# Optimization experiments

Hardware: AMD Instinct MI355X
Metric: run time of the kernel (lower is better)

The kernel has to match this reference:

```python
import jax, jax.numpy as jnp
import numpy as np

H = 256  # hidden_size == in_size
M = int(H * 4 / 3)  # 341, gated-MLP intermediate
EPS = 1e-5


def _layer_norm(x, w, b):
    mu = jnp.mean(x, axis=-1, keepdims=True)
    var = jnp.var(x, axis=-1, keepdims=True)
    return (x - mu) * jax.lax.rsqrt(var + EPS) * w + b


def setup_inputs() -> dict:
    key = jax.random.key(0)
    ks = jax.random.split(key, 8)
    s = 0.02
    inp = {
        "x": jax.random.normal(ks[0], (64, 2048, H), dtype=jnp.float32),
        "ln1_w": jnp.ones((H,), jnp.float32),
        "ln1_b": jnp.zeros((H,), jnp.float32),
        # sLSTM: stacked [z, i, f, o] input and recurrent weights
        "W": jax.random.normal(ks[1], (4 * H, H), jnp.float32) * s,
        "R": jax.random.normal(ks[2], (4 * H, H), jnp.float32) * s,
        "b": jnp.zeros((4 * H,), jnp.float32),
        "up_W": jax.random.normal(ks[3], (M, H), jnp.float32) * s,
        "up_b": jnp.zeros((M,), jnp.float32),
        "gate_W": jax.random.normal(ks[4], (M, H), jnp.float32) * s,
        "gate_b": jnp.zeros((M,), jnp.float32),
        "down_W": jax.random.normal(ks[5], (H, M), jnp.float32) * s,
        "down_b": jnp.zeros((H,), jnp.float32),
        "ln2_w": jnp.ones((H,), jnp.float32),
        "ln2_b": jnp.zeros((H,), jnp.float32),
    }
    return inp


def _slstm(nx, W, R, b):
    # nx: (B, T, H) -> all hidden states (B, T, H)
    B, T, _ = nx.shape
    xW = jnp.einsum("bth,gh->btg", nx, W) + b  # (B, T, 4H)
    xW = jnp.swapaxes(xW, 0, 1)  # (T, B, 4H)

    def step(carry, xw_t):
        h, c, n, m = carry  # each (B, H)
        pre = xw_t + h @ R.T
        z = jnp.tanh(pre[:, :H])
        log_i = pre[:, H:2 * H]
        log_f = pre[:, 2 * H:3 * H]
        o = jax.nn.sigmoid(pre[:, 3 * H:])
        m_new = jnp.maximum(log_f + m, log_i)  # stabilizer
        i_g = jnp.exp(log_i - m_new)
        f_g = jnp.exp(log_f + m - m_new)
        c = f_g * c + i_g * z
        n = f_g * n + i_g
        h = o * (c / n)
        return (h, c, n, m_new), h

    z0 = jnp.zeros((B, H), nx.dtype)
    (_, _, _, _), hs = jax.lax.scan(step, (z0, z0, z0, z0), xW)
    return jnp.swapaxes(hs, 0, 1)  # (B, T, H)


def reference(x, ln1_w, ln1_b, W, R, b, up_W, up_b, gate_W, gate_b,
              down_W, down_b, ln2_w, ln2_b):
    residual = x
    nx = _layer_norm(x, ln1_w, ln1_b)
    lstm_out = _slstm(nx, W, R, b)
    gate_signal = jax.nn.gelu(jnp.einsum("bth,mh->btm", lstm_out, gate_W) + gate_b)
    mlp_inter = jnp.einsum("bth,mh->btm", lstm_out, up_W) + up_b
    mlp_out = jnp.einsum("btm,hm->bth", gate_signal * mlp_inter, down_W) + down_b
    return _layer_norm(mlp_out, ln2_w, ln2_b) + residual
```

## Files before the change

### kernel.cpp

```cpp
#include <hip/hip_runtime.h>
#include <hip/hip_bf16.h>
#include <hip/hip_fp16.h>

typedef _Float16 f16;
typedef __hip_bfloat16 bf16;
typedef short bf16x8 __attribute__((ext_vector_type(8)));
typedef float f32x4 __attribute__((ext_vector_type(4)));
typedef int i32x4 __attribute__((ext_vector_type(4)));
typedef _Float16 f16x2 __attribute__((ext_vector_type(2)));

#define HDIM 256
#define G4   1024
#define TT   2048
#define NB   64
#define NTOK (64*2048)
#define MPAD 384

__device__ __forceinline__ float gelu_tanh(float x) {
    float x3 = x*x*x;
    float t = tanhf(0.7978845608028654f * (x + 0.044715f * x3));
    return 0.5f * x * (1.0f + t);
}

__global__ void k_prep_w(const float* __restrict__ W, bf16* __restrict__ Wb) {
    int i = blockIdx.x*256 + threadIdx.x;
    Wb[i] = __float2bfloat16(W[i]);
}

__global__ __launch_bounds__(256) void k_prep_r8(const float* __restrict__ R,
        char* __restrict__ R8, float* __restrict__ rscale) {
    int wave = threadIdx.x >> 6, lane = threadIdx.x & 63;
    int g = blockIdx.x*4 + wave;
    float4 v = ((const float4*)(R + (long)g*256))[lane];
    float mx = fmaxf(fmaxf(fabsf(v.x), fabsf(v.y)), fmaxf(fabsf(v.z), fabsf(v.w)));
    #pragma unroll
    for (int m = 1; m < 64; m <<= 1) mx = fmaxf(mx, __shfl_xor(mx, m, 64));
    float inv = (mx > 0.f) ? 127.f/mx : 0.f;
    int q0 = (int)rintf(v.x*inv), q1 = (int)rintf(v.y*inv);
    int q2 = (int)rintf(v.z*inv), q3 = (int)rintf(v.w*inv);
    unsigned packed = (q0 & 0xff) | ((q1 & 0xff) << 8) | ((q2 & 0xff) << 16) | ((q3 & 0xff) << 24);
    ((unsigned*)(R8 + (long)g*256))[lane] = packed;
    if (lane == 0) rscale[g] = mx * (1.0f/127.f);
}

__global__ void k_prep_gu(const float* __restrict__ gW, const float* __restrict__ uW,
                          const float* __restrict__ gb, const float* __restrict__ ub,
                          bf16* __restrict__ gWb, bf16* __restrict__ uWb,
                          float* __restrict__ gbp, float* __restrict__ ubp) {
    int i = blockIdx.x*256 + threadIdx.x;
    int r = i >> 8, c = i & 255;
    gWb[i] = __float2bfloat16(r < 341 ? gW[r*256 + c] : 0.f);
    uWb[i] = __float2bfloat16(r < 341 ? uW[r*256 + c] : 0.f);
    if (i < 384) {
        gbp[i] = i < 341 ? gb[i] : 0.f;
        ubp[i] = i < 341 ? ub[i] : 0.f;
    }
}

__global__ void k_prep_down(const float* __restrict__ dW, bf16* __restrict__ dWb) {
    int i = blockIdx.x*256 + threadIdx.x;
    int r = i / 384, c = i % 384;
    dWb[i] = __float2bfloat16(c < 341 ? dW[r*341 + c] : 0.f);
}

__global__ __launch_bounds__(256) void k_ln1(const float* __restrict__ x,
        const float* __restrict__ w, const float* __restrict__ b,
        bf16* __restrict__ nx) {
    int wave = threadIdx.x >> 6, lane = threadIdx.x & 63;
    long tok = (long)blockIdx.x * 4 + wave;
    float4 v = ((const float4*)(x + tok*HDIM))[lane];
    float s = v.x + v.y + v.z + v.w;
    float q = v.x*v.x + v.y*v.y + v.z*v.z + v.w*v.w;
    #pragma unroll
    for (int m = 1; m < 64; m <<= 1) { s += __shfl_xor(s, m, 64); q += __shfl_xor(q, m, 64); }
    float mean = s * (1.0f/HDIM);
    float rs = rsqrtf(q*(1.0f/HDIM) - mean*mean + 1e-5f);
    float4 wv = ((const float4*)w)[lane];
    float4 bv = ((const float4*)b)[lane];
    bf16 tmp[4];
    tmp[0] = __float2bfloat16((v.x-mean)*rs*wv.x + bv.x);
    tmp[1] = __float2bfloat16((v.y-mean)*rs*wv.y + bv.y);
    tmp[2] = __float2bfloat16((v.z-mean)*rs*wv.z + bv.z);
    tmp[3] = __float2bfloat16((v.w-mean)*rs*wv.w + bv.w);
    *(ushort4*)(nx + tok*HDIM + lane*4) = *(ushort4*)tmp;
}

__global__ __launch_bounds__(256) void k_ln2(const f16* __restrict__ mlp,
        const float* __restrict__ x, const float* __restrict__ w,
        const float* __restrict__ b, float* __restrict__ out) {
    int wave = threadIdx.x >> 6, lane = threadIdx.x & 63;
    long tok = (long)blockIdx.x * 4 + wave;
    const f16* mr = mlp + tok*HDIM + lane*4;
    float4 v; v.x = (float)mr[0]; v.y = (float)mr[1]; v.z = (float)mr[2]; v.w = (float)mr[3];
    float s = v.x + v.y + v.z + v.w;
    float q = v.x*v.x + v.y*v.y + v.z*v.z + v.w*v.w;
    #pragma unroll
    for (int m = 1; m < 64; m <<= 1) { s += __shfl_xor(s, m, 64); q += __shfl_xor(q, m, 64); }
    float mean = s * (1.0f/HDIM);
    float rs = rsqrtf(q*(1.0f/HDIM) - mean*mean + 1e-5f);
    float4 wv = ((const float4*)w)[lane];
    float4 bv = ((const float4*)b)[lane];
    float4 xv = ((const float4*)(x + tok*HDIM))[lane];
    float4 ov;
    ov.x = (v.x-mean)*rs*wv.x + bv.x + xv.x;
    ov.y = (v.y-mean)*rs*wv.y + bv.y + xv.y;
    ov.z = (v.z-mean)*rs*wv.z + bv.z + xv.z;
    ov.w = (v.w-mean)*rs*wv.w + bv.w + xv.w;
    ((float4*)(out + tok*HDIM))[lane] = ov;
}

enum { MODE_F16 = 0, MODE_GELU_F16 = 1, MODE_MUL_BF16 = 2, MODE_XW_F16 = 3 };

template<int MODE>
__global__ __launch_bounds__(256) void k_gemm(
    const bf16* __restrict__ A, const bf16* __restrict__ Bm,
    const float* __restrict__ bias, void* __restrict__ Cv,
    const f16* __restrict__ gatebuf,
    int K, int lda, int ldb, int ldc, int ldg)
{
    __shared__ char Al[128*128];
    __shared__ char Bl[64*128];
    const int tid = threadIdx.x;
    const long bm = (long)blockIdx.x * 128;
    const int bn = blockIdx.y * 64;
    const int wave = tid >> 6, lane = tid & 63;
    const int wm = wave >> 1, wn = wave & 1;
    const int l16 = lane & 15, lq = lane >> 4;
    f32x4 acc[4][2] = {};
    for (int k0 = 0; k0 < K; k0 += 64) {
        #pragma unroll
        for (int p = 0; p < 4; ++p) {
            int ci = tid + p*256;
            int row = ci >> 3, s = ci & 7;
            uint4 d = *(const uint4*)(A + (bm + row)*lda + k0 + s*8);
            *(uint4*)(Al + row*128 + ((s ^ (row&7))<<4)) = d;
        }
        #pragma unroll
        for (int p = 0; p < 2; ++p) {
            int ci = tid + p*256;
            int row = ci >> 3, s = ci & 7;
            uint4 d = *(const uint4*)(Bm + (long)(bn + row)*ldb + k0 + s*8);
            *(uint4*)(Bl + row*128 + ((s ^ (row&7))<<4)) = d;
        }
        __syncthreads();
        #pragma unroll
        for (int kc = 0; kc < 2; ++kc) {
            bf16x8 bf[2];
            #pragma unroll
            for (int fn = 0; fn < 2; ++fn) {
                int row = wn*32 + fn*16 + l16;
                int slot = (kc<<2) + lq;
                bf[fn] = *(const bf16x8*)(Bl + row*128 + ((slot ^ (row&7))<<4));
            }
            #pragma unroll
            for (int fm = 0; fm < 4; ++fm) {
                int row = wm*64 + fm*16 + l16;
                int slot = (kc<<2) + lq;
                bf16x8 af = *(const bf16x8*)(Al + row*128 + ((slot ^ (row&7))<<4));
                acc[fm][0] = __builtin_amdgcn_mfma_f32_16x16x32_bf16(af, bf[0], acc[fm][0], 0,0,0);
                acc[fm][1] = __builtin_amdgcn_mfma_f32_16x16x32_bf16(af, bf[1], acc[fm][1], 0,0,0);
            }
        }
        __syncthreads();
    }
    #pragma unroll
    for (int fm = 0; fm < 4; ++fm) {
        #pragma unroll
        for (int fn = 0; fn < 2; ++fn) {
            int n = bn + wn*32 + fn*16 + l16;
            float bv = bias[n];
            #pragma unroll
            for (int r = 0; r < 4; ++r) {
                long m = bm + wm*64 + fm*16 + lq*4 + r;
                float v = acc[fm][fn][r] + bv;
                if constexpr (MODE == MODE_F16) {
                    ((f16*)Cv)[m*ldc + n] = (f16)v;
                } else if constexpr (MODE == MODE_XW_F16) {
                    ((f16*)Cv)[m*ldc + ((n & 255) << 2) + (n >> 8)] = (f16)v;
                } else if constexpr (MODE == MODE_GELU_F16) {
                    ((f16*)Cv)[m*ldc + n] = (f16)gelu_tanh(v);
                } else {
                    float g = (float)gatebuf[m*ldg + n];
                    ((bf16*)Cv)[m*ldc + n] = __float2bfloat16(g * v);
                }
            }
        }
    }
}


__global__ __launch_bounds__(1024) __attribute__((amdgpu_waves_per_eu(4, 4)))
void k_scan(const f16* __restrict__ xW, const char* __restrict__ R8,
            const float* __restrict__ rscale, bf16* __restrict__ h_out)
{
    __shared__ char hq[2][256];
    const int tid = threadIdx.x;
    const int b    = blockIdx.x;
    const int w    = tid >> 6;
    const int lane = tid & 63;
    const int c    = lane & 15;
    const int q    = lane >> 4;
    const int j    = w*16 + c;

    uint4 Bf[4][4];
    #pragma unroll
    for (int m = 0; m < 4; ++m) {
        #pragma unroll
        for (int kk = 0; kk < 4; ++kk)
            Bf[m][kk] = *(const uint4*)(R8 + (long)(j + 256*m)*256 + kk*64 + q*16);
    }
    float rs[4];
    #pragma unroll
    for (int m = 0; m < 4; ++m)
        rs[m] = rscale[j + 256*m] * (1.0f/127.0f);
    if (tid < 64) ((unsigned*)hq[0])[tid] = 0u;

    const char* xg = (const char*)xW + (long)b * TT * 2048 + j*8;
    bf16* hrow = h_out + (long)b * TT * HDIM;

    uint2 XA = *(const uint2*)(xg);
    uint2 XB = *(const uint2*)(xg + 2048);
    float cst = 0.f, nst = 0.f, mst = 0.f;
    int cur = 0;
    __syncthreads();

#define SCAN_STEP(XREG, TPRE)                                                   \
    do {                                                                        \
        f16x2 xlo = __builtin_bit_cast(f16x2, XREG.x);                          \
        f16x2 xhi = __builtin_bit_cast(f16x2, XREG.y);                          \
        XREG = *(const uint2*)(xg + (long)(TPRE)*2048);                         \
        i32x4 af[4];                                                            \
        _Pragma("unroll")                                                       \
        for (int kk = 0; kk < 4; ++kk)                                          \
            af[kk] = __builtin_bit_cast(i32x4,                                  \
                         *(const uint4*)(hq[cur] + kk*64 + q*16));              \
        i32x4 ac0 = {0,0,0,0}, ac1 = {0,0,0,0}, ac2 = {0,0,0,0}, ac3 = {0,0,0,0}; \
        _Pragma("unroll")                                                       \
        for (int kk = 0; kk < 4; ++kk) {                                        \
            ac0 = __builtin_amdgcn_mfma_i32_16x16x64_i8(af[kk], __builtin_bit_cast(i32x4, Bf[0][kk]), ac0, 0,0,0); \
            ac1 = __builtin_amdgcn_mfma_i32_16x16x64_i8(af[kk], __builtin_bit_cast(i32x4, Bf[1][kk]), ac1, 0,0,0); \
            ac2 = __builtin_amdgcn_mfma_i32_16x16x64_i8(af[kk], __builtin_bit_cast(i32x4, Bf[2][kk]), ac2, 0,0,0); \
            ac3 = __builtin_amdgcn_mfma_i32_16x16x64_i8(af[kk], __builtin_bit_cast(i32x4, Bf[3][kk]), ac3, 0,0,0); \
        }                                                                       \
        float pz = rs[0]*(float)ac0[0] + (float)xlo[0];                         \
        float pi = rs[1]*(float)ac1[0] + (float)xlo[1];                         \
        float pf = rs[2]*(float)ac2[0] + (float)xhi[0];                         \
        float po = rs[3]*(float)ac3[0] + (float)xhi[1];                         \
        float e = __expf(-2.0f * fabsf(pz));                                    \
        float z = copysignf((1.0f - e) / (1.0f + e), pz);                       \
        float o = 1.0f / (1.0f + __expf(-po));                                  \
        float mn = fmaxf(pf + mst, pi);                                         \
        float ig = __expf(pi - mn);                                             \
        float fg = __expf(pf + mst - mn);                                       \
        cst = fg*cst + ig*z;                                                    \
        nst = fg*nst + ig;                                                      \
        mst = mn;                                                               \
        float h = o * (cst / nst);                                              \
        if (q == 0) {                                                           \
            hq[cur^1][j] = (char)(int)rintf(h * 127.f);                         \
            hrow[j] = __float2bfloat16(h);                                      \
        }                                                                       \
        __builtin_amdgcn_sched_barrier(0);                                      \
        asm volatile("s_waitcnt lgkmcnt(0)" ::: "memory");                      \
        __builtin_amdgcn_s_barrier();                                           \
        __builtin_amdgcn_sched_barrier(0);                                      \
        cur ^= 1;                                                               \
        hrow += HDIM;                                                           \
    } while (0)

    for (int t = 0; t < TT; t += 2) {
        SCAN_STEP(XA, t + 2);
        SCAN_STEP(XB, t + 3);
    }
#undef SCAN_STEP
}

extern "C" void kernel_launch(void* const* d_in, const int* in_sizes, int n_in,
                              void* d_out, int out_size, void* d_ws, size_t ws_size,
                              hipStream_t stream) {
    const float* x     = (const float*)d_in[0];
    const float* ln1w  = (const float*)d_in[1];
    const float* ln1b  = (const float*)d_in[2];
    const float* W     = (const float*)d_in[3];
    const float* R     = (const float*)d_in[4];
    const float* bg    = (const float*)d_in[5];
    const float* upW   = (const float*)d_in[6];
    const float* upb   = (const float*)d_in[7];
    const float* gateW = (const float*)d_in[8];
    const float* gateb = (const float*)d_in[9];
    const float* downW = (const float*)d_in[10];
    const float* downb = (const float*)d_in[11];
    const float* ln2w  = (const float*)d_in[12];
    const float* ln2b  = (const float*)d_in[13];

    char* ws = (char*)d_ws;
    size_t off = 0;
    auto alloc = [&](size_t bytes) { char* p = ws + off; off += (bytes + 255) & ~255ULL; return p; };
    f16*  mlp16   = (f16*)alloc((size_t)NTOK*HDIM*2);
    char* regionB = alloc((size_t)NTOK*G4*2);
    bf16* h       = (bf16*)alloc((size_t)NTOK*HDIM*2);
    bf16* Wb      = (bf16*)alloc(262144*2);
    char* R8      = (char*)alloc(262144);
    float* rscale = (float*)alloc(1024*4);
    bf16* gWb     = (bf16*)alloc((size_t)MPAD*256*2);
    bf16* uWb     = (bf16*)alloc((size_t)MPAD*256*2);
    bf16* dWb     = (bf16*)alloc((size_t)256*MPAD*2);
    float* gbp    = (float*)alloc(MPAD*4);
    float* ubp    = (float*)alloc(MPAD*4);

    bf16* nx       = (bf16*)mlp16;
    f16*  xWb      = (f16*)regionB;
    f16*  gate_out = (f16*)regionB;
    bf16* prod     = (bf16*)(regionB + (size_t)NTOK*MPAD*2);

    k_prep_w   <<<1024, 256, 0, stream>>>(W, Wb);
    k_prep_r8  <<<256, 256, 0, stream>>>(R, R8, rscale);
    k_prep_gu  <<<384, 256, 0, stream>>>(gateW, upW, gateb, upb, gWb, uWb, gbp, ubp);
    k_prep_down<<<384, 256, 0, stream>>>(downW, dWb);
    k_ln1      <<<NTOK/4, 256, 0, stream>>>(x, ln1w, ln1b, nx);
    k_gemm<MODE_XW_F16><<<dim3(1024, 16), 256, 0, stream>>>(nx, Wb, bg, xWb, nullptr, 256, 256, 256, 1024, 0);
    k_scan     <<<64, 1024, 0, stream>>>(xWb, R8, rscale, h);
    k_gemm<MODE_GELU_F16><<<dim3(1024, 6), 256, 0, stream>>>(h, gWb, gbp, gate_out, nullptr, 256, 256, 256, MPAD, 0);
    k_gemm<MODE_MUL_BF16><<<dim3(1024, 6), 256, 0, stream>>>(h, uWb, ubp, prod, gate_out, 256, 256, 256, MPAD, MPAD);
    k_gemm<MODE_F16><<<dim3(1024, 4), 256, 0, stream>>>(prod, dWb, downb, mlp16, nullptr, MPAD, MPAD, MPAD, HDIM, 0);
    k_ln2      <<<NTOK/4, 256, 0, stream>>>(mlp16, x, ln2w, ln2b, (float*)d_out);
}
```

Before: 2.566 ms.

## Split scan recurrent matvec between MFMA waves and VALU dot4 waves

The recurrent int8 matvec in the sLSTM scan is now divided within each block. Waves 0-7 compute hidden units 0-127 with int8 MFMA as before. Waves 8-15 compute units 128-255 with VALU sdot4 instructions and a DPP quad reduction, and MFMA sections get raised priority via setprio. The aim is to relieve contention on the shared matrix unit, since all 16 waves previously issued MFMAs every step and the per-step latency is the critical path. The cost is that the VALU half may be slower per step, and since both halves meet at a barrier every step, the slower path sets the pace.

```diff
diff --git a/kernel.cpp b/kernel.cpp
--- a/kernel.cpp
+++ b/kernel.cpp
@@ -15,6 +15,27 @@
 #define NB   64
 #define NTOK (64*2048)
 #define MPAD 384
+
+__device__ __forceinline__ int dot4i(unsigned a, unsigned b, int c) {
+#if __has_builtin(__builtin_amdgcn_sdot4)
+    return __builtin_amdgcn_sdot4((int)a, (int)b, c, false);
+#else
+    char4 x = __builtin_bit_cast(char4, a), y = __builtin_bit_cast(char4, b);
+    return c + (int)x.x*(int)y.x + (int)x.y*(int)y.y + (int)x.z*(int)y.z + (int)x.w*(int)y.w;
+#endif
+}
+
+__device__ __forceinline__ int quad_red(int v) {
+#if __has_builtin(__builtin_amdgcn_update_dpp)
+    v += __builtin_amdgcn_update_dpp(0, v, 0xB1, 0xF, 0xF, true);
+    v += __builtin_amdgcn_update_dpp(0, v, 0x4E, 0xF, 0xF, true);
+    return v;
+#else
+    v += __shfl_xor(v, 1, 64);
+    v += __shfl_xor(v, 2, 64);
+    return v;
+#endif
+}
 
 __device__ __forceinline__ float gelu_tanh(float x) {
     float x3 = x*x*x;
@@ -189,63 +210,11 @@
 }
 
 
-__global__ __launch_bounds__(1024) __attribute__((amdgpu_waves_per_eu(4, 4)))
-void k_scan(const f16* __restrict__ xW, const char* __restrict__ R8,
-            const float* __restrict__ rscale, bf16* __restrict__ h_out)
-{
-    __shared__ char hq[2][256];
-    const int tid = threadIdx.x;
-    const int b    = blockIdx.x;
-    const int w    = tid >> 6;
-    const int lane = tid & 63;
-    const int c    = lane & 15;
-    const int q    = lane >> 4;
-    const int j    = w*16 + c;
-
-    uint4 Bf[4][4];
-    #pragma unroll
-    for (int m = 0; m < 4; ++m) {
-        #pragma unroll
-        for (int kk = 0; kk < 4; ++kk)
-            Bf[m][kk] = *(const uint4*)(R8 + (long)(j + 256*m)*256 + kk*64 + q*16);
-    }
-    float rs[4];
-    #pragma unroll
-    for (int m = 0; m < 4; ++m)
-        rs[m] = rscale[j + 256*m] * (1.0f/127.0f);
-    if (tid < 64) ((unsigned*)hq[0])[tid] = 0u;
-
-    const char* xg = (const char*)xW + (long)b * TT * 2048 + j*8;
-    bf16* hrow = h_out + (long)b * TT * HDIM;
-
-    uint2 XA = *(const uint2*)(xg);
-    uint2 XB = *(const uint2*)(xg + 2048);
-    float cst = 0.f, nst = 0.f, mst = 0.f;
-    int cur = 0;
-    __syncthreads();
-
-#define SCAN_STEP(XREG, TPRE)                                                   \
-    do {                                                                        \
-        f16x2 xlo = __builtin_bit_cast(f16x2, XREG.x);                          \
-        f16x2 xhi = __builtin_bit_cast(f16x2, XREG.y);                          \
-        XREG = *(const uint2*)(xg + (long)(TPRE)*2048);                         \
-        i32x4 af[4];                                                            \
-        _Pragma("unroll")                                                       \
-        for (int kk = 0; kk < 4; ++kk)                                          \
-            af[kk] = __builtin_bit_cast(i32x4,                                  \
-                         *(const uint4*)(hq[cur] + kk*64 + q*16));              \
-        i32x4 ac0 = {0,0,0,0}, ac1 = {0,0,0,0}, ac2 = {0,0,0,0}, ac3 = {0,0,0,0}; \
-        _Pragma("unroll")                                                       \
-        for (int kk = 0; kk < 4; ++kk) {                                        \
-            ac0 = __builtin_amdgcn_mfma_i32_16x16x64_i8(af[kk], __builtin_bit_cast(i32x4, Bf[0][kk]), ac0, 0,0,0); \
-            ac1 = __builtin_amdgcn_mfma_i32_16x16x64_i8(af[kk], __builtin_bit_cast(i32x4, Bf[1][kk]), ac1, 0,0,0); \
-            ac2 = __builtin_amdgcn_mfma_i32_16x16x64_i8(af[kk], __builtin_bit_cast(i32x4, Bf[2][kk]), ac2, 0,0,0); \
-            ac3 = __builtin_amdgcn_mfma_i32_16x16x64_i8(af[kk], __builtin_bit_cast(i32x4, Bf[3][kk]), ac3, 0,0,0); \
-        }                                                                       \
-        float pz = rs[0]*(float)ac0[0] + (float)xlo[0];                         \
-        float pi = rs[1]*(float)ac1[0] + (float)xlo[1];                         \
-        float pf = rs[2]*(float)ac2[0] + (float)xhi[0];                         \
-        float po = rs[3]*(float)ac3[0] + (float)xhi[1];                         \
+#define SLSTM_EPI_PUB(S0v, S1v, S2v, S3v, XREG)                                 \
+        float pz = rs[0]*(float)(S0v) + (float)__builtin_bit_cast(f16x2, XREG.x)[0]; \
+        float pi = rs[1]*(float)(S1v) + (float)__builtin_bit_cast(f16x2, XREG.x)[1]; \
+        float pf = rs[2]*(float)(S2v) + (float)__builtin_bit_cast(f16x2, XREG.y)[0]; \
+        float po = rs[3]*(float)(S3v) + (float)__builtin_bit_cast(f16x2, XREG.y)[1]; \
         float e = __expf(-2.0f * fabsf(pz));                                    \
         float z = copysignf((1.0f - e) / (1.0f + e), pz);                       \
         float o = 1.0f / (1.0f + __expf(-po));                                  \
@@ -256,7 +225,7 @@
         nst = fg*nst + ig;                                                      \
         mst = mn;                                                               \
         float h = o * (cst / nst);                                              \
-        if (q == 0) {                                                           \
+        if (pub) {                                                              \
             hq[cur^1][j] = (char)(int)rintf(h * 127.f);                         \
             hrow[j] = __float2bfloat16(h);                                      \
         }                                                                       \
@@ -265,14 +234,126 @@
         __builtin_amdgcn_s_barrier();                                           \
         __builtin_amdgcn_sched_barrier(0);                                      \
         cur ^= 1;                                                               \
-        hrow += HDIM;                                                           \
+        hrow += HDIM;
+
+__global__ __launch_bounds__(1024) __attribute__((amdgpu_waves_per_eu(4, 4)))
+void k_scan(const f16* __restrict__ xW, const char* __restrict__ R8,
+            const float* __restrict__ rscale, bf16* __restrict__ h_out)
+{
+    __shared__ char hq[2][256];
+    const int tid = threadIdx.x;
+    const int b    = blockIdx.x;
+    const int w    = tid >> 6;
+    const int lane = tid & 63;
+
+    if (tid < 64) ((unsigned*)hq[0])[tid] = 0u;
+    __syncthreads();
+
+    const char* xg0 = (const char*)xW + (long)b * TT * 2048;
+    bf16* hrow = h_out + (long)b * TT * HDIM;
+
+    if (w < 8) {
+        const int c = lane & 15;
+        const int q = lane >> 4;
+        const int j = w*16 + c;
+        const bool pub = (q == 0);
+
+        uint4 Bf[4][4];
+        #pragma unroll
+        for (int m = 0; m < 4; ++m)
+            #pragma unroll
+            for (int kk = 0; kk < 4; ++kk)
+                Bf[m][kk] = *(const uint4*)(R8 + (long)(j + 256*m)*256 + kk*64 + q*16);
+        float rs[4];
+        #pragma unroll
+        for (int m = 0; m < 4; ++m)
+            rs[m] = rscale[j + 256*m] * (1.0f/127.0f);
+
+        const char* xg = xg0 + j*8;
+        uint2 XA = *(const uint2*)(xg);
+        uint2 XB = *(const uint2*)(xg + 2048);
+        float cst = 0.f, nst = 0.f, mst = 0.f;
+        int cur = 0;
+
+#define STEP_MFMA(XREG, TPRE)                                                   \
+    do {                                                                        \
+        uint2 Xc = XREG;                                                        \
+        XREG = *(const uint2*)(xg + (long)(TPRE)*2048);                         \
+        i32x4 af[4];                                                            \
+        _Pragma("unroll")                                                       \
+        for (int kk = 0; kk < 4; ++kk)                                          \
+            af[kk] = __builtin_bit_cast(i32x4,                                  \
+                         *(const uint4*)(hq[cur] + kk*64 + q*16));              \
+        i32x4 ac0 = {0,0,0,0}, ac1 = {0,0,0,0}, ac2 = {0,0,0,0}, ac3 = {0,0,0,0}; \
+        __builtin_amdgcn_s_setprio(1);                                          \
+        _Pragma("unroll")                                                       \
+        for (int kk = 0; kk < 4; ++kk) {                                        \
+            ac0 = __builtin_amdgcn_mfma_i32_16x16x64_i8(af[kk], __builtin_bit_cast(i32x4, Bf[0][kk]), ac0, 0,0,0); \
+            ac1 = __builtin_amdgcn_mfma_i32_16x16x64_i8(af[kk], __builtin_bit_cast(i32x4, Bf[1][kk]), ac1, 0,0,0); \
+            ac2 = __builtin_amdgcn_mfma_i32_16x16x64_i8(af[kk], __builtin_bit_cast(i32x4, Bf[2][kk]), ac2, 0,0,0); \
+            ac3 = __builtin_amdgcn_mfma_i32_16x16x64_i8(af[kk], __builtin_bit_cast(i32x4, Bf[3][kk]), ac3, 0,0,0); \
+        }                                                                       \
+        __builtin_amdgcn_s_setprio(0);                                          \
+        SLSTM_EPI_PUB(ac0[0], ac1[0], ac2[0], ac3[0], Xc)                       \
     } while (0)
 
-    for (int t = 0; t < TT; t += 2) {
-        SCAN_STEP(XA, t + 2);
-        SCAN_STEP(XB, t + 3);
+        for (int t = 0; t < TT; t += 2) {
+            STEP_MFMA(XA, t + 2);
+            STEP_MFMA(XB, t + 3);
+        }
+#undef STEP_MFMA
+    } else {
+        const int kg = lane & 3;
+        const int jj = lane >> 2;
+        const int j = 128 + (w - 8)*16 + jj;
+        const bool pub = (kg == 0);
+
+        uint4 Rq[4][4];
+        #pragma unroll
+        for (int m = 0; m < 4; ++m)
+            #pragma unroll
+            for (int i = 0; i < 4; ++i)
+                Rq[m][i] = *(const uint4*)(R8 + (long)(j + 256*m)*256 + kg*64 + i*16);
+        float rs[4];
+        #pragma unroll
+        for (int m = 0; m < 4; ++m)
+            rs[m] = rscale[j + 256*m] * (1.0f/127.0f);
+
+        const char* xg = xg0 + j*8;
+        uint2 XA = *(const uint2*)(xg);
+        uint2 XB = *(const uint2*)(xg + 2048);
+        float cst = 0.f, nst = 0.f, mst = 0.f;
+        int cur = 0;
+
+#define STEP_VALU(XREG, TPRE)                                                   \
+    do {                                                                        \
+        uint2 Xc = XREG;                                                        \
+        XREG = *(const uint2*)(xg + (long)(TPRE)*2048);                         \
+        int S0 = 0, S1 = 0, S2 = 0, S3 = 0;                                     \
+        _Pragma("unroll")                                                       \
+        for (int i = 0; i < 4; ++i) {                                           \
+            uint4 hv = *(const uint4*)(hq[cur] + kg*64 + i*16);                 \
+            uint4 r0 = Rq[0][i], r1 = Rq[1][i], r2 = Rq[2][i], r3 = Rq[3][i];   \
+            S0 = dot4i(r0.x, hv.x, S0); S0 = dot4i(r0.y, hv.y, S0);             \
+            S0 = dot4i(r0.z, hv.z, S0); S0 = dot4i(r0.w, hv.w, S0);             \
+            S1 = dot4i(r1.x, hv.x, S1); S1 = dot4i(r1.y, hv.y, S1);             \
+            S1 = dot4i(r1.z, hv.z, S1); S1 = dot4i(r1.w, hv.w, S1);             \
+            S2 = dot4i(r2.x, hv.x, S2); S2 = dot4i(r2.y, hv.y, S2);             \
+            S2 = dot4i(r2.z, hv.z, S2); S2 = dot4i(r2.w, hv.w, S2);             \
+            S3 = dot4i(r3.x, hv.x, S3); S3 = dot4i(r3.y, hv.y, S3);             \
+            S3 = dot4i(r3.z, hv.z, S3); S3 = dot4i(r3.w, hv.w, S3);             \
+        }                                                                       \
+        S0 = quad_red(S0); S1 = quad_red(S1);                                   \
+        S2 = quad_red(S2); S3 = quad_red(S3);                                   \
+        SLSTM_EPI_PUB(S0, S1, S2, S3, Xc)                                       \
+    } while (0)
+
+        for (int t = 0; t < TT; t += 2) {
+            STEP_VALU(XA, t + 2);
+            STEP_VALU(XB, t + 3);
+        }
+#undef STEP_VALU
     }
-#undef SCAN_STEP
 }
 
 extern "C" void kernel_launch(void* const* d_in, const int* in_sizes, int n_in,
```

Result: slower. 2.844 ms (+10.8%).
